# Kernel optimization log

Measured on AMD Instinct MI355X. Metric: run time of the kernel, lower is better.

## Reference

```python
import jax, jax.numpy as jnp
import numpy as np

# ---- module constants (from init_kwargs) ----
N_DIM = 2                      # n: latent dim (len(active_dims))
T_STEPS = 100                  # t: linspace(0,1,t) integration grid
M_PER_DIM = 12                 # m = [12,12] HSGP basis per dim
C_FACTOR = 1.5                 # c: HSGP domain expansion factor
X_EXTENT = 3.0                 # data extent (x0 ~ N(0,1) lives in [-3,3])
L_BOUND = C_FACTOR * X_EXTENT  # HSGP half-domain length L = c*S
D_COMPS = N_DIM * (N_DIM + 1) // 2  # d = 3 metric components

# eigen-index grid over all dim combinations: [M_TOTAL, n]
_J = np.stack(np.meshgrid(*[np.arange(1, M_PER_DIM + 1)] * N_DIM, indexing='ij'), -1)
J = jnp.asarray(_J.reshape(-1, N_DIM).astype(np.float32))
M_TOTAL = J.shape[0]
_r, _c = np.triu_indices(N_DIM)
ROWS, COLS = jnp.asarray(_r), jnp.asarray(_c)

# explicit Adams-Bashforth coefficients (orders 1..4), newest derivative first
AB_COEFFS = jnp.array([
    [1.0, 0.0, 0.0, 0.0],
    [1.5, -0.5, 0.0, 0.0],
    [23.0/12.0, -16.0/12.0, 5.0/12.0, 0.0],
    [55.0/24.0, -59.0/24.0, 37.0/24.0, -9.0/24.0]], dtype=jnp.float32)


def hsgp_features(x, ls, alpha):
    """HSGP ExpQuad linearized basis phi(x) and its spatial derivative dphi.
    x: [B, n] -> phi: [B, M], dphi: [B, M, n]."""
    w = jnp.pi * J / (2.0 * L_BOUND)                  # [M, n] per-dim frequencies
    arg = w[None] * (x[:, None, :] + L_BOUND)         # [B, M, n]
    s, c = jnp.sin(arg), jnp.cos(arg)
    norm = L_BOUND ** (-0.5 * N_DIM)
    phi = norm * jnp.prod(s, axis=-1)                 # [B, M]
    dcols = []
    for i in range(N_DIM):                            # structural loop over n=2 dims
        p = w[None, :, i] * c[:, :, i]
        for j2 in range(N_DIM):
            if j2 != i:
                p = p * s[:, :, j2]
        dcols.append(norm * p)
    dphi = jnp.stack(dcols, axis=-1)                  # [B, M, n]
    # ExpQuad spectral density sqrt weights
    S = (alpha ** 2) * ((2.0 * jnp.pi) ** (0.5 * N_DIM)) * jnp.prod(ls) \
        * jnp.exp(-0.5 * jnp.sum((ls ** 2)[None] * w ** 2, axis=-1))  # [M]
    sq = jnp.sqrt(S)
    return phi * sq[None], dphi * sq[None, :, None]


def geodesic_rhs(y, beta, ls, alpha):
    """geomstats-style geodesic equation: y = stack([x, v]) -> stack([v, a]),
    a^k = -Gamma^k_{ij} v^i v^j with GP-parameterized Christoffels."""
    x, v = y[0], y[1]                                 # [B, n]
    B = x.shape[0]
    phi, dphi = hsgp_features(x, ls, alpha)
    f = phi @ beta.T                                  # [B, d] metric components
    df = jnp.einsum('bmi,dm->bdi', dphi, beta)        # [B, d, n] their derivatives
    G = jnp.zeros((B, N_DIM, N_DIM), x.dtype)
    G = G.at[:, ROWS, COLS].set(f).at[:, COLS, ROWS].set(f)
    G = G + jnp.eye(N_DIM, dtype=x.dtype)             # identity offset keeps G invertible
    D = jnp.zeros((B, N_DIM, N_DIM, N_DIM), x.dtype)  # D[b,l,j,i] = d_i g_{lj}
    D = D.at[:, ROWS, COLS, :].set(df).at[:, COLS, ROWS, :].set(df)
    Ginv = jnp.linalg.inv(G)
    # term[b,l,i,j] = d_i g_{lj} + d_j g_{li} - d_l g_{ij}
    term = jnp.transpose(D, (0, 1, 3, 2)) + D - jnp.transpose(D, (0, 3, 1, 2))
    Gam = 0.5 * jnp.einsum('bkl,blij->bkij', Ginv, term)
    acc = -jnp.einsum('bkij,bi,bj->bk', Gam, v, v)
    return jnp.stack([v, acc])


def adams_integrate(y0, beta, ls, alpha, rhs):
    """Fixed-grid explicit Adams (order<=4, lower-order startup) over linspace(0,1,t)."""
    h = jnp.float32(1.0 / (T_STEPS - 1))
    hist0 = jnp.zeros((4,) + y0.shape, y0.dtype)
    def step(carry, idx):
        y, hist = carry
        fcur = rhs(y, beta, ls, alpha)
        hist = jnp.concatenate([fcur[None], hist[:-1]], axis=0)  # newest first
        coef = AB_COEFFS[jnp.minimum(idx, 3)]
        y_next = y + h * jnp.tensordot(coef, hist, axes=1)
        return (y_next, hist), y_next
    _, ys = jax.lax.scan(step, (y0, hist0), jnp.arange(T_STEPS - 1))
    return jnp.concatenate([y0[None], ys], axis=0)    # [t, 2, B, n]


def setup_inputs():
    key = jax.random.key(0)
    k1, k2, k3, k4 = jax.random.split(key, 4)
    B = 50000
    x0 = jax.random.normal(k1, (B, N_DIM), jnp.float32)
    v0 = 0.2 * jax.random.normal(k2, (B, N_DIM), jnp.float32)
    beta = 0.05 * jax.random.normal(k3, (D_COMPS, M_TOTAL), jnp.float32)
    ls = 0.3 + 0.5 * jax.random.uniform(k4, (N_DIM,), jnp.float32)
    alpha = jnp.float32(1.0)
    return {"x0": x0, "v0": v0, "beta": beta, "ls": ls, "alpha": alpha}


def reference(x0, v0, beta, ls, alpha):
    y0 = jnp.stack([x0, v0])                          # [2, B, n]
    return adams_integrate(y0, beta, ls, alpha, geodesic_rhs)
```

## Files before the change

kernel.cpp:

```cpp
#include <hip/hip_runtime.h>
#include <math.h>

typedef _Float16 h4 __attribute__((ext_vector_type(4)));
typedef float    f4 __attribute__((ext_vector_type(4)));

namespace {
constexpr float LB = 4.5f;
constexpr float WF = (float)M_PI / (2.0f * LB);
}

__global__ void setup_A_kernel(const float* __restrict__ beta,
                               const float* __restrict__ ls,
                               const float* __restrict__ alpha,
                               _Float16* __restrict__ A) {
    int idx = blockIdx.x * blockDim.x + threadIdx.x;
    if (idx >= 768) return;
    int d = idx >> 8;
    int l = (idx >> 2) & 63;
    int t = idx & 3;
    int r = l & 15;
    int k = ((l >> 4) << 2) + t;
    float val = 0.0f;
    if (r < 12 && k < 12) {
        float w0 = WF * (float)(r + 1);
        float w1 = WF * (float)(k + 1);
        float l0 = ls[0], l1 = ls[1], al = alpha[0];
        float S = al * al * (2.0f * (float)M_PI) * l0 * l1 *
                  expf(-0.5f * (l0 * l0 * w0 * w0 + l1 * l1 * w1 * w1));
        val = beta[d * 144 + r * 12 + k] * sqrtf(S) * (1.0f / LB);
    }
    A[idx] = (_Float16)val;
}

__device__ __forceinline__ void trig4(float th, float mb, float* s, float* c) {
    float s1 = __sinf(th), c1 = __cosf(th);
    float sb = __sinf(mb * th), cb = __cosf(mb * th);
    s[0] = sb; c[0] = cb;
    #pragma unroll
    for (int t = 1; t < 4; ++t) {
        s[t] = fmaf(s[t - 1], c1,  c[t - 1] * s1);
        c[t] = fmaf(c[t - 1], c1, -(s[t - 1] * s1));
    }
}

__global__ __launch_bounds__(256)
void geo_kernel(const float* __restrict__ xg, const float* __restrict__ vg,
                const _Float16* Ag ,
                float* __restrict__ out, int B)
{
    int lane = threadIdx.x & 63;
    int wave = (blockIdx.x * 256 + threadIdx.x) >> 6;
    int ebase = wave << 4;
    if (ebase >= B) return;
    int g = lane >> 4;
    int e = ebase + (lane & 15);
    if (e >= B) e = B - 1;

    union U8 { uint2 u; h4 h; };
    const uint2* Au = reinterpret_cast<const uint2*>(Ag);
    U8 a0, a1, a2;
    a0.u = Au[0 * 64 + lane];
    a1.u = Au[1 * 64 + lane];
    a2.u = Au[2 * 64 + lane];
    asm volatile("" ::: "memory");
    h4 A0 = a0.h, A1 = a1.h, A2 = a2.h;

    float mb = (float)(4 * g + 1);
    float Wm[4];
    #pragma unroll
    for (int t = 0; t < 4; ++t) Wm[t] = WF * (mb + (float)t);

    float2 xv = reinterpret_cast<const float2*>(xg)[e];
    float2 vv2 = reinterpret_cast<const float2*>(vg)[e];
    float x0 = xv.x, x1 = xv.y, v0 = vv2.x, v1 = vv2.y;

    unsigned off = 4u * ((((unsigned)(g >> 1) * (unsigned)B) + (unsigned)e) * 2u
                         + (unsigned)(g & 1));
    const unsigned stride = 16u * (unsigned)B;
    char* outc = reinterpret_cast<char*>(out);
    {
        float sval = (g & 2) ? ((g & 1) ? v1 : v0) : ((g & 1) ? x1 : x0);
        *reinterpret_cast<float*>(outc + off) = sval;
    }

    float h1x = 0.f, h2x = 0.f, h3x = 0.f, h1y = 0.f, h2y = 0.f, h3y = 0.f;
    float g1x = 0.f, g2x = 0.f, g3x = 0.f, g1y = 0.f, g2y = 0.f, g3y = 0.f;
    const float h = 1.0f / 99.0f;

    auto STEP = [&](float c0, float c1c, float c2c, float c3c) {
        float s0v[4], c0v[4], s1v[4], c1v[4], wc0[4];
        trig4(WF * (x0 + LB), mb, s0v, c0v);
        trig4(WF * (x1 + LB), mb, s1v, c1v);
        #pragma unroll
        for (int t = 0; t < 4; ++t) wc0[t] = Wm[t] * c0v[t];

        h4 bs, bc;
        #pragma unroll
        for (int t = 0; t < 4; ++t) {
            bs[t] = (_Float16)s1v[t];
            bc[t] = (_Float16)(Wm[t] * c1v[t]);
        }

        f4 z = {0.f, 0.f, 0.f, 0.f};
        f4 u0 = __builtin_amdgcn_mfma_f32_16x16x16f16(A0, bs, z, 0, 0, 0);
        f4 u1 = __builtin_amdgcn_mfma_f32_16x16x16f16(A1, bs, z, 0, 0, 0);
        f4 u2 = __builtin_amdgcn_mfma_f32_16x16x16f16(A2, bs, z, 0, 0, 0);
        f4 w0 = __builtin_amdgcn_mfma_f32_16x16x16f16(A0, bc, z, 0, 0, 0);
        f4 w1 = __builtin_amdgcn_mfma_f32_16x16x16f16(A1, bc, z, 0, 0, 0);
        f4 w2 = __builtin_amdgcn_mfma_f32_16x16x16f16(A2, bc, z, 0, 0, 0);

        float f0 = 0.f, f1 = 0.f, f2 = 0.f;
        float dA0 = 0.f, dA1 = 0.f, dA2 = 0.f;
        float dB0 = 0.f, dB1 = 0.f, dB2 = 0.f;
        #pragma unroll
        for (int t = 0; t < 4; ++t) {
            float sA = s0v[t], cA = wc0[t];
            f0  = fmaf(sA, u0[t], f0);   dA0 = fmaf(cA, u0[t], dA0);
            f1  = fmaf(sA, u1[t], f1);   dA1 = fmaf(cA, u1[t], dA1);
            f2  = fmaf(sA, u2[t], f2);   dA2 = fmaf(cA, u2[t], dA2);
            dB0 = fmaf(sA, w0[t], dB0);
            dB1 = fmaf(sA, w1[t], dB1);
            dB2 = fmaf(sA, w2[t], dB2);
        }

        float vv00 = v0 * v0, vv01 = v0 * v1, vv11 = v1 * v1;
        float q0p = dA0 * vv00 + 2.0f * dB0 * vv01 + fmaf(2.0f, dB1, -dA2) * vv11;
        float q1p = fmaf(2.0f, dA1, -dB0) * vv00 + 2.0f * dA2 * vv01 + dB2 * vv11;

        f0  += __shfl_xor(f0, 16);  f0  += __shfl_xor(f0, 32);
        f1  += __shfl_xor(f1, 16);  f1  += __shfl_xor(f1, 32);
        f2  += __shfl_xor(f2, 16);  f2  += __shfl_xor(f2, 32);
        q0p += __shfl_xor(q0p, 16); q0p += __shfl_xor(q0p, 32);
        q1p += __shfl_xor(q1p, 16); q1p += __shfl_xor(q1p, 32);

        float G00 = f0 + 1.0f, G01 = f1, G11 = f2 + 1.0f;
        float det = fmaf(G00, G11, -(G01 * G01));
        float rdet = __builtin_amdgcn_rcpf(det);
        float a0v = -0.5f * rdet * fmaf(G11, q0p, -(G01 * q1p));
        float a1v = -0.5f * rdet * fmaf(G00, q1p, -(G01 * q0p));

        float dx0 = fmaf(c0, v0, fmaf(c1c, h1x, fmaf(c2c, h2x, c3c * h3x)));
        float dx1 = fmaf(c0, v1, fmaf(c1c, h1y, fmaf(c2c, h2y, c3c * h3y)));
        float dv0 = fmaf(c0, a0v, fmaf(c1c, g1x, fmaf(c2c, g2x, c3c * g3x)));
        float dv1 = fmaf(c0, a1v, fmaf(c1c, g1y, fmaf(c2c, g2y, c3c * g3y)));
        h3x = h2x; h2x = h1x; h1x = v0;  h3y = h2y; h2y = h1y; h1y = v1;
        g3x = g2x; g2x = g1x; g1x = a0v; g3y = g2y; g2y = g1y; g1y = a1v;
        x0 = fmaf(h, dx0, x0); x1 = fmaf(h, dx1, x1);
        v0 = fmaf(h, dv0, v0); v1 = fmaf(h, dv1, v1);

        off += stride;
        float sval = (g & 2) ? ((g & 1) ? v1 : v0) : ((g & 1) ? x1 : x0);
        *reinterpret_cast<float*>(outc + off) = sval;
    };

    STEP(1.0f, 0.0f, 0.0f, 0.0f);
    STEP(1.5f, -0.5f, 0.0f, 0.0f);
    STEP(23.0f / 12.0f, -16.0f / 12.0f, 5.0f / 12.0f, 0.0f);
    #pragma unroll 2
    for (int t = 3; t < 99; ++t)
        STEP(55.0f / 24.0f, -59.0f / 24.0f, 37.0f / 24.0f, -9.0f / 24.0f);
}

extern "C" void kernel_launch(void* const* d_in, const int* in_sizes, int n_in,
                              void* d_out, int out_size, void* d_ws, size_t ws_size,
                              hipStream_t stream) {
    const float* x0    = (const float*)d_in[0];
    const float* v0    = (const float*)d_in[1];
    const float* beta  = (const float*)d_in[2];
    const float* ls    = (const float*)d_in[3];
    const float* alpha = (const float*)d_in[4];
    float* out = (float*)d_out;
    _Float16* A = (_Float16*)d_ws;

    int B = in_sizes[0] / 2;

    hipLaunchKernelGGL(setup_A_kernel, dim3(12), dim3(64), 0, stream,
                       beta, ls, alpha, A);

    int waves = (B + 15) / 16;
    int grid  = (waves + 3) / 4;
    hipLaunchKernelGGL(geo_kernel, dim3(grid), dim3(256), 0, stream,
                       x0, v0, A, out, B);
}
```

Before: 139.2 us.

## Use permlane swaps for cross-group reduction, packed f16 converts, one-wave blocks

The cross-group reductions switch from __shfl_xor (ds_bpermute through LDS hardware) to v_permlane16_swap/v_permlane32_swap register swaps, which avoids LDS-path latency on each of the 99 serial steps. The f16 conversions for the MFMA B operand use packed cvt_pkrtz, which rounds toward zero instead of to nearest. Blocks shrink from 256 to 64 threads (one wave each), giving finer-grained scheduling and better tail balance, and the main loop unroll rises from 2 to 4, which may raise register pressure.

```diff
diff --git a/kernel.cpp b/kernel.cpp
--- a/kernel.cpp
+++ b/kernel.cpp
@@ -2,6 +2,7 @@
 #include <math.h>
 
 typedef _Float16 h4 __attribute__((ext_vector_type(4)));
+typedef _Float16 h2 __attribute__((ext_vector_type(2)));
 typedef float    f4 __attribute__((ext_vector_type(4)));
 
 namespace {
@@ -43,14 +44,28 @@
     }
 }
 
-__global__ __launch_bounds__(256)
+__device__ __forceinline__ h4 pack4(float a, float b, float c, float d) {
+    h2 lo = __builtin_bit_cast(h2, __builtin_amdgcn_cvt_pkrtz(a, b));
+    h2 hi = __builtin_bit_cast(h2, __builtin_amdgcn_cvt_pkrtz(c, d));
+    return __builtin_shufflevector(lo, hi, 0, 1, 2, 3);
+}
+
+__device__ __forceinline__ float cross_sum4(float x) {
+    float a = x, b = x;
+    asm("v_permlane16_swap_b32 %0, %1" : "+v"(a), "+v"(b));
+    float s = a + b;
+    float c = s, d = s;
+    asm("v_permlane32_swap_b32 %0, %1" : "+v"(c), "+v"(d));
+    return c + d;
+}
+
+__global__ __launch_bounds__(64)
 void geo_kernel(const float* __restrict__ xg, const float* __restrict__ vg,
                 const _Float16* Ag ,
                 float* __restrict__ out, int B)
 {
-    int lane = threadIdx.x & 63;
-    int wave = (blockIdx.x * 256 + threadIdx.x) >> 6;
-    int ebase = wave << 4;
+    int lane = threadIdx.x;
+    int ebase = blockIdx.x << 4;
     if (ebase >= B) return;
     int g = lane >> 4;
     int e = ebase + (lane & 15);
@@ -94,12 +109,9 @@
         #pragma unroll
         for (int t = 0; t < 4; ++t) wc0[t] = Wm[t] * c0v[t];
 
-        h4 bs, bc;
-        #pragma unroll
-        for (int t = 0; t < 4; ++t) {
-            bs[t] = (_Float16)s1v[t];
-            bc[t] = (_Float16)(Wm[t] * c1v[t]);
-        }
+        h4 bs = pack4(s1v[0], s1v[1], s1v[2], s1v[3]);
+        h4 bc = pack4(Wm[0] * c1v[0], Wm[1] * c1v[1],
+                      Wm[2] * c1v[2], Wm[3] * c1v[3]);
 
         f4 z = {0.f, 0.f, 0.f, 0.f};
         f4 u0 = __builtin_amdgcn_mfma_f32_16x16x16f16(A0, bs, z, 0, 0, 0);
@@ -127,11 +139,11 @@
         float q0p = dA0 * vv00 + 2.0f * dB0 * vv01 + fmaf(2.0f, dB1, -dA2) * vv11;
         float q1p = fmaf(2.0f, dA1, -dB0) * vv00 + 2.0f * dA2 * vv01 + dB2 * vv11;
 
-        f0  += __shfl_xor(f0, 16);  f0  += __shfl_xor(f0, 32);
-        f1  += __shfl_xor(f1, 16);  f1  += __shfl_xor(f1, 32);
-        f2  += __shfl_xor(f2, 16);  f2  += __shfl_xor(f2, 32);
-        q0p += __shfl_xor(q0p, 16); q0p += __shfl_xor(q0p, 32);
-        q1p += __shfl_xor(q1p, 16); q1p += __shfl_xor(q1p, 32);
+        f0  = cross_sum4(f0);
+        f1  = cross_sum4(f1);
+        f2  = cross_sum4(f2);
+        q0p = cross_sum4(q0p);
+        q1p = cross_sum4(q1p);
 
         float G00 = f0 + 1.0f, G01 = f1, G11 = f2 + 1.0f;
         float det = fmaf(G00, G11, -(G01 * G01));
@@ -156,7 +168,7 @@
     STEP(1.0f, 0.0f, 0.0f, 0.0f);
     STEP(1.5f, -0.5f, 0.0f, 0.0f);
     STEP(23.0f / 12.0f, -16.0f / 12.0f, 5.0f / 12.0f, 0.0f);
-    #pragma unroll 2
+    #pragma unroll 4
     for (int t = 3; t < 99; ++t)
         STEP(55.0f / 24.0f, -59.0f / 24.0f, 37.0f / 24.0f, -9.0f / 24.0f);
 }
@@ -177,8 +189,7 @@
     hipLaunchKernelGGL(setup_A_kernel, dim3(12), dim3(64), 0, stream,
                        beta, ls, alpha, A);
 
-    int waves = (B + 15) / 16;
-    int grid  = (waves + 3) / 4;
-    hipLaunchKernelGGL(geo_kernel, dim3(grid), dim3(256), 0, stream,
+    int grid = (B + 15) / 16;
+    hipLaunchKernelGGL(geo_kernel, dim3(grid), dim3(64), 0, stream,
                        x0, v0, A, out, B);
 }
```

After: 151.4 us. +8.7%, slower.
